# Performance work log

Hardware: AMD Instinct MI355X
Metric: run time of the kernel (lower is better)

## Reference

```python
import jax, jax.numpy as jnp
import numpy as np

H_LAT = 64   # latent height (original_shape H)
W_LAT = 64   # latent width  (original_shape W)
COND_LEN = 77  # text tokens per regional condition


def _resize_nearest_exact(m, H, W):
    # matches torch F.interpolate(mode='nearest-exact') for a 2D mask
    h0, w0 = m.shape
    ih = jnp.floor((jnp.arange(H) + 0.5) * (h0 / H)).astype(jnp.int32)
    iw = jnp.floor((jnp.arange(W) + 0.5) * (w0 / W)).astype(jnp.int32)
    return m[ih][:, iw]


def setup_inputs() -> dict:
    key = jax.random.key(0)
    kq, kk, kv, km = jax.random.split(key, 4)
    b, qlen, inner = 2, H_LAT * W_LAT, 512
    klen = 4 * COND_LEN  # 4 regions x 77 tokens
    q = jax.random.normal(kq, (b, qlen, inner), dtype=jnp.float32)
    k = jax.random.normal(kk, (b, klen, inner), dtype=jnp.float32)
    v = jax.random.normal(kv, (b, klen, inner), dtype=jnp.float32)
    dd_masks = jax.random.uniform(km, (4, 32, 32), dtype=jnp.float32)
    # ensure full spatial coverage (region 0 = global) so no softmax row is all-masked
    dd_masks = dd_masks.at[0].set(1.0)
    return {"q": q, "k": k, "v": v, "dd_masks": dd_masks, "heads": 8}


def reference(q, k, v, dd_masks, heads):
    b, qlen, inner = q.shape
    dh = inner // heads
    # [b, heads, seq, dh]
    qh = q.reshape(b, qlen, heads, dh).transpose(0, 2, 1, 3)
    kh = k.reshape(b, -1, heads, dh).transpose(0, 2, 1, 3)
    vh = v.reshape(b, -1, heads, dh).transpose(0, 2, 1, 3)

    # build DenseDiffusion mask: each region mask resized to HxW, flattened,
    # and repeated over that region's COND_LEN key columns
    R = dd_masks.shape[0]
    resized = jax.vmap(lambda m: _resize_nearest_exact(m, H_LAT, W_LAT))(dd_masks)  # [R,H,W]
    flat = resized.reshape(R, H_LAT * W_LAT).T            # [HW, R]
    masks = jnp.repeat(flat, COND_LEN, axis=1)            # [HW, R*COND_LEN]
    mask_bool = masks > 0.5                               # [HW, klen]
    mask_scale = (H_LAT * W_LAT) / jnp.sum(masks, axis=0, keepdims=True)  # [1, klen]

    scale = 1.0 / np.sqrt(dh).astype(np.float32)
    attn = jnp.einsum('bhqd,bhkd->bhqk', qh, kh) * scale  # [b,h,HW,klen]
    attn = attn * mask_scale                              # broadcast over b,h,q
    attn = jnp.where(mask_bool, attn, -jnp.inf)
    w = jax.nn.softmax(attn, axis=-1)
    out = jnp.einsum('bhqk,bhkd->bhqd', w, vh)
    return out.transpose(0, 2, 1, 3).reshape(b, qlen, heads * dh)
```

## Files before the change

### kernel.cpp

```cpp
#include <hip/hip_runtime.h>
#include <hip/hip_bf16.h>

typedef __attribute__((ext_vector_type(8))) short short8;
typedef __attribute__((ext_vector_type(4))) float floatx4;

#define HW_TOK 4096
#define KLEN 308
#define DH 64
#define INNER 512

#define KROWS 320
#define VSTRU 328
#define VBASE (KROWS * 64)
#define KV_TOTAL (VBASE + DH * VSTRU)
#define PSTR 40
#define NWAVES 16

__device__ __forceinline__ unsigned short f2bf(float f) {
    union { float f; unsigned u; } x; x.f = f;
    unsigned u = x.u;
    return (unsigned short)((u + 0x7FFFu + ((u >> 16) & 1u)) >> 16);
}
__device__ __forceinline__ unsigned pk2bf(float a, float b) {
    return ((unsigned)f2bf(b) << 16) | (unsigned)f2bf(a);
}

__global__ __launch_bounds__(1024, 1)
void dd_attn_kernel(const float* __restrict__ q,
                    const float* __restrict__ k,
                    const float* __restrict__ v,
                    const float* __restrict__ dd,
                    float* __restrict__ out) {
    __shared__ unsigned short KV[KV_TOTAL];
    __shared__ unsigned short Pb[NWAVES][16][PSTR];

    const int tid  = threadIdx.x;
    const int lane = tid & 63;
    const int wave = tid >> 6;
    const int quad = lane >> 4;
    const int l15  = lane & 15;

    const int bid = blockIdx.x;
    const int bh  = bid >> 4;
    const int grp = bid & 15;
    const int b = bh >> 3, h = bh & 7;

    const float* qp = q + (size_t)b * HW_TOK * INNER + h * DH;
    const float* kp = k + (size_t)b * KLEN * INNER + h * DH;
    const float* vp = v + (size_t)b * KLEN * INNER + h * DH;
    float* op = out + (size_t)b * HW_TOK * INNER + h * DH;

    for (int e = tid; e < KLEN * 32; e += 1024) {
        int row = e >> 5, d2 = e & 31;
        float2 f = *(const float2*)(kp + (size_t)row * INNER + 2 * d2);
        int c = d2 >> 2;
        int off = row * 64 + (((c ^ (row & 7)) << 3) | ((d2 & 3) << 1));
        *(unsigned*)&KV[off] = pk2bf(f.x, f.y);
    }
    for (int e = tid; e < 12 * 64; e += 1024) KV[KLEN * 64 + e] = 0;

    #pragma unroll
    for (int i = 0; i < 3; ++i) {
        int cq = wave + NWAVES * i;
        if (cq < 40) {
            float f[8];
            #pragma unroll
            for (int j = 0; j < 8; ++j) {
                int col = cq * 8 + j;
                f[j] = (col < KLEN) ? vp[(size_t)col * INNER + lane] : 0.f;
            }
            union { short8 s; unsigned u[4]; } vv;
            #pragma unroll
            for (int j = 0; j < 4; ++j) vv.u[j] = pk2bf(f[2 * j], f[2 * j + 1]);
            int swz = (cq & ~7) | ((cq ^ (lane & 7)) & 7);
            *(short8*)&KV[VBASE + lane * VSTRU + (swz << 3)] = vv.s;
        }
    }
    float rsum = 0.f;
    {
        const float* dp = dd + quad * 1024 + l15 * 4;
        #pragma unroll
        for (int j = 0; j < 16; ++j) {
            float4 f = *(const float4*)(dp + j * 64);
            rsum += f.x + f.y + f.z + f.w;
        }
        #pragma unroll
        for (int off = 1; off < 16; off <<= 1) rsum += __shfl_xor(rsum, off);
    }
    float rsc[4];
    #pragma unroll
    for (int r = 0; r < 4; ++r)
        rsc[r] = 4096.0f / (4.0f * __shfl(rsum, r * 16 + l15));

    __syncthreads();

    const int q0 = (grp * NWAVES + wave) * 16;
    const int qrow = q0 + l15;

    const float* qr = qp + (size_t)qrow * INNER + quad * 8;
    float4 g0 = *(const float4*)(qr);
    float4 g1 = *(const float4*)(qr + 4);
    float4 g2 = *(const float4*)(qr + 32);
    float4 g3 = *(const float4*)(qr + 36);
    short8 qa0, qa1;
    {
        union { short8 s; unsigned u[4]; } ua, ub;
        ua.u[0] = pk2bf(g0.x, g0.y); ua.u[1] = pk2bf(g0.z, g0.w);
        ua.u[2] = pk2bf(g1.x, g1.y); ua.u[3] = pk2bf(g1.z, g1.w);
        ub.u[0] = pk2bf(g2.x, g2.y); ub.u[1] = pk2bf(g2.z, g2.w);
        ub.u[2] = pk2bf(g3.x, g3.y); ub.u[3] = pk2bf(g3.z, g3.w);
        qa0 = ua.s; qa1 = ub.s;
    }

    const int mi = (qrow >> 7) * 32 + ((qrow & 63) >> 1);
    float coef[4];
    #pragma unroll
    for (int r = 0; r < 4; ++r)
        coef[r] = (dd[r * 1024 + mi] > 0.5f) ? 0.125f * rsc[r] : -1.0f;

    float m_run = -INFINITY, l_run = 0.f;
    floatx4 oacc[4] = {{0,0,0,0},{0,0,0,0},{0,0,0,0},{0,0,0,0}};

    #pragma unroll
    for (int ch = 0; ch < 4; ++ch) {
        const int NT = (ch < 3) ? 6 : 2;
        floatx4 acc[6];

        #pragma unroll
        for (int t = 0; t < NT; ++t) {
            int row = (ch * 6 + t) * 16 + l15;
            short8 ka0 = *(const short8*)&KV[row * 64 + (((quad    ) ^ (row & 7)) << 3)];
            short8 ka1 = *(const short8*)&KV[row * 64 + (((4 + quad) ^ (row & 7)) << 3)];
            floatx4 c = {0.f, 0.f, 0.f, 0.f};
            c = __builtin_amdgcn_mfma_f32_16x16x32_bf16(ka0, qa0, c, 0, 0, 0);
            c = __builtin_amdgcn_mfma_f32_16x16x32_bf16(ka1, qa1, c, 0, 0, 0);
            acc[t] = c;
        }

        float mloc = -INFINITY;
        #pragma unroll
        for (int t = 0; t < NT; ++t) {
            #pragma unroll
            for (int r = 0; r < 4; ++r) {
                int kc = (ch * 6 + t) * 16 + quad * 4 + r;
                float cf = (kc < 77) ? coef[0] : (kc < 154) ? coef[1]
                         : (kc < 231) ? coef[2] : (kc < 308) ? coef[3] : -1.0f;
                float sv = (cf > 0.f) ? acc[t][r] * cf : -INFINITY;
                acc[t][r] = sv;
                mloc = fmaxf(mloc, sv);
            }
        }
        mloc = fmaxf(mloc, __shfl_xor(mloc, 16));
        mloc = fmaxf(mloc, __shfl_xor(mloc, 32));
        float m_new = fmaxf(m_run, mloc);
        float alpha = __expf(m_run - m_new);
        float lloc = 0.f;
        #pragma unroll
        for (int t = 0; t < NT; ++t) {
            #pragma unroll
            for (int r = 0; r < 4; ++r) {
                float p = __expf(acc[t][r] - m_new);
                acc[t][r] = p;
                lloc += p;
            }
        }
        lloc += __shfl_xor(lloc, 16);
        lloc += __shfl_xor(lloc, 32);
        l_run = l_run * alpha + lloc;
        m_run = m_new;
        #pragma unroll
        for (int n = 0; n < 4; ++n)
            #pragma unroll
            for (int r = 0; r < 4; ++r) oacc[n][r] *= alpha;

        const int NS = NT / 2;
        #pragma unroll
        for (int s = 0; s < NS; ++s) {
            unsigned p0 = pk2bf(acc[2*s][0],   acc[2*s][1]);
            unsigned p1 = pk2bf(acc[2*s][2],   acc[2*s][3]);
            unsigned p2 = pk2bf(acc[2*s+1][0], acc[2*s+1][1]);
            unsigned p3 = pk2bf(acc[2*s+1][2], acc[2*s+1][3]);
            *(uint2*)&Pb[wave][l15][quad * 4]      = make_uint2(p0, p1);
            *(uint2*)&Pb[wave][l15][16 + quad * 4] = make_uint2(p2, p3);
            short8 pbv = *(const short8*)&Pb[wave][l15][quad * 8];
            #pragma unroll
            for (int n = 0; n < 4; ++n) {
                int row = n * 16 + l15;
                int cq = ch * 12 + s * 4 + quad;
                int swz = (cq & ~7) | ((cq ^ (row & 7)) & 7);
                short8 va = *(const short8*)&KV[VBASE + row * VSTRU + (swz << 3)];
                oacc[n] = __builtin_amdgcn_mfma_f32_16x16x32_bf16(va, pbv, oacc[n], 0, 0, 0);
            }
        }
    }

    const float inv = 1.0f / l_run;
    float* o = op + (size_t)qrow * INNER + quad * 4;
    #pragma unroll
    for (int n = 0; n < 4; ++n) {
        float4 ov;
        ov.x = oacc[n][0] * inv;
        ov.y = oacc[n][1] * inv;
        ov.z = oacc[n][2] * inv;
        ov.w = oacc[n][3] * inv;
        *(float4*)&o[n * 16] = ov;
    }
}

extern "C" void kernel_launch(void* const* d_in, const int* in_sizes, int n_in,
                              void* d_out, int out_size, void* d_ws, size_t ws_size,
                              hipStream_t stream) {
    const float* q  = (const float*)d_in[0];
    const float* k  = (const float*)d_in[1];
    const float* v  = (const float*)d_in[2];
    const float* dd = (const float*)d_in[3];
    float* out = (float*)d_out;
    dd_attn_kernel<<<dim3(256), dim3(1024), 0, stream>>>(q, k, v, dd, out);
}
```

Before: 93.19 us.

## Switch attention to 32x32x16 MFMA tiles with 8 waves of 32 queries

Moves both the QK^T and PV products from 16x16x32 to 32x32x16 bf16 MFMA. Each wave now handles 32 query rows and 160-key chunks (two chunks instead of four), and the block shrinks to 512 threads. The aim is fewer MFMA issues and LDS reads per unit of work, plus fewer online-softmax rescale steps and cross-lane shuffles. In exchange, per-wave register use grows (16-wide accumulators), and the last chunk computes over 12 padded zero keys. Fewer waves per block also means less latency hiding during the K/V staging.

```diff
diff --git a/kernel.cpp b/kernel.cpp
--- a/kernel.cpp
+++ b/kernel.cpp
@@ -2,7 +2,7 @@
 #include <hip/hip_bf16.h>
 
 typedef __attribute__((ext_vector_type(8))) short short8;
-typedef __attribute__((ext_vector_type(4))) float floatx4;
+typedef __attribute__((ext_vector_type(16))) float floatx16;
 
 #define HW_TOK 4096
 #define KLEN 308
@@ -13,8 +13,8 @@
 #define VSTRU 328
 #define VBASE (KROWS * 64)
 #define KV_TOTAL (VBASE + DH * VSTRU)
-#define PSTR 40
-#define NWAVES 16
+#define PSTRU 40
+#define NW 8
 
 __device__ __forceinline__ unsigned short f2bf(float f) {
     union { float f; unsigned u; } x; x.f = f;
@@ -25,18 +25,20 @@
     return ((unsigned)f2bf(b) << 16) | (unsigned)f2bf(a);
 }
 
-__global__ __launch_bounds__(1024, 1)
+__global__ __launch_bounds__(512, 1)
 void dd_attn_kernel(const float* __restrict__ q,
                     const float* __restrict__ k,
                     const float* __restrict__ v,
                     const float* __restrict__ dd,
                     float* __restrict__ out) {
     __shared__ unsigned short KV[KV_TOTAL];
-    __shared__ unsigned short Pb[NWAVES][16][PSTR];
+    __shared__ unsigned short Pb[NW][32][PSTRU];
 
     const int tid  = threadIdx.x;
     const int lane = tid & 63;
     const int wave = tid >> 6;
+    const int half = lane >> 5;
+    const int l31  = lane & 31;
     const int quad = lane >> 4;
     const int l15  = lane & 15;
 
@@ -50,31 +52,29 @@
     const float* vp = v + (size_t)b * KLEN * INNER + h * DH;
     float* op = out + (size_t)b * HW_TOK * INNER + h * DH;
 
-    for (int e = tid; e < KLEN * 32; e += 1024) {
+    for (int e = tid; e < KLEN * 32; e += 512) {
         int row = e >> 5, d2 = e & 31;
         float2 f = *(const float2*)(kp + (size_t)row * INNER + 2 * d2);
         int c = d2 >> 2;
         int off = row * 64 + (((c ^ (row & 7)) << 3) | ((d2 & 3) << 1));
         *(unsigned*)&KV[off] = pk2bf(f.x, f.y);
     }
-    for (int e = tid; e < 12 * 64; e += 1024) KV[KLEN * 64 + e] = 0;
-
-    #pragma unroll
-    for (int i = 0; i < 3; ++i) {
-        int cq = wave + NWAVES * i;
-        if (cq < 40) {
-            float f[8];
-            #pragma unroll
-            for (int j = 0; j < 8; ++j) {
-                int col = cq * 8 + j;
-                f[j] = (col < KLEN) ? vp[(size_t)col * INNER + lane] : 0.f;
-            }
-            union { short8 s; unsigned u[4]; } vv;
-            #pragma unroll
-            for (int j = 0; j < 4; ++j) vv.u[j] = pk2bf(f[2 * j], f[2 * j + 1]);
-            int swz = (cq & ~7) | ((cq ^ (lane & 7)) & 7);
-            *(short8*)&KV[VBASE + lane * VSTRU + (swz << 3)] = vv.s;
-        }
+    for (int e = tid; e < 12 * 64; e += 512) KV[KLEN * 64 + e] = 0;
+
+    #pragma unroll
+    for (int i = 0; i < 5; ++i) {
+        int cq = wave + NW * i;
+        float f[8];
+        #pragma unroll
+        for (int j = 0; j < 8; ++j) {
+            int col = cq * 8 + j;
+            f[j] = (col < KLEN) ? vp[(size_t)col * INNER + lane] : 0.f;
+        }
+        union { short8 s; unsigned u[4]; } vv;
+        #pragma unroll
+        for (int j = 0; j < 4; ++j) vv.u[j] = pk2bf(f[2 * j], f[2 * j + 1]);
+        int swz = (cq & ~7) | ((cq ^ (lane & 7)) & 7);
+        *(short8*)&KV[VBASE + lane * VSTRU + (swz << 3)] = vv.s;
     }
     float rsum = 0.f;
     {
@@ -94,22 +94,20 @@
 
     __syncthreads();
 
-    const int q0 = (grp * NWAVES + wave) * 16;
-    const int qrow = q0 + l15;
-
-    const float* qr = qp + (size_t)qrow * INNER + quad * 8;
-    float4 g0 = *(const float4*)(qr);
-    float4 g1 = *(const float4*)(qr + 4);
-    float4 g2 = *(const float4*)(qr + 32);
-    float4 g3 = *(const float4*)(qr + 36);
-    short8 qa0, qa1;
-    {
-        union { short8 s; unsigned u[4]; } ua, ub;
-        ua.u[0] = pk2bf(g0.x, g0.y); ua.u[1] = pk2bf(g0.z, g0.w);
-        ua.u[2] = pk2bf(g1.x, g1.y); ua.u[3] = pk2bf(g1.z, g1.w);
-        ub.u[0] = pk2bf(g2.x, g2.y); ub.u[1] = pk2bf(g2.z, g2.w);
-        ub.u[2] = pk2bf(g3.x, g3.y); ub.u[3] = pk2bf(g3.z, g3.w);
-        qa0 = ua.s; qa1 = ub.s;
+    const int q0 = (grp * NW + wave) * 32;
+    const int qrow = q0 + l31;
+
+    short8 qb[4];
+    const float* qr = qp + (size_t)qrow * INNER;
+    #pragma unroll
+    for (int ks = 0; ks < 4; ++ks) {
+        const float* p0 = qr + ks * 16 + half * 8;
+        float4 a = *(const float4*)p0;
+        float4 c = *(const float4*)(p0 + 4);
+        union { short8 s; unsigned u[4]; } u;
+        u.u[0] = pk2bf(a.x, a.y); u.u[1] = pk2bf(a.z, a.w);
+        u.u[2] = pk2bf(c.x, c.y); u.u[3] = pk2bf(c.z, c.w);
+        qb[ks] = u.s;
     }
 
     const int mi = (qrow >> 7) * 32 + ((qrow & 63) >> 1);
@@ -119,91 +117,113 @@
         coef[r] = (dd[r * 1024 + mi] > 0.5f) ? 0.125f * rsc[r] : -1.0f;
 
     float m_run = -INFINITY, l_run = 0.f;
-    floatx4 oacc[4] = {{0,0,0,0},{0,0,0,0},{0,0,0,0},{0,0,0,0}};
-
-    #pragma unroll
-    for (int ch = 0; ch < 4; ++ch) {
-        const int NT = (ch < 3) ? 6 : 2;
-        floatx4 acc[6];
-
-        #pragma unroll
-        for (int t = 0; t < NT; ++t) {
-            int row = (ch * 6 + t) * 16 + l15;
-            short8 ka0 = *(const short8*)&KV[row * 64 + (((quad    ) ^ (row & 7)) << 3)];
-            short8 ka1 = *(const short8*)&KV[row * 64 + (((4 + quad) ^ (row & 7)) << 3)];
-            floatx4 c = {0.f, 0.f, 0.f, 0.f};
-            c = __builtin_amdgcn_mfma_f32_16x16x32_bf16(ka0, qa0, c, 0, 0, 0);
-            c = __builtin_amdgcn_mfma_f32_16x16x32_bf16(ka1, qa1, c, 0, 0, 0);
+    floatx16 oacc[2];
+    #pragma unroll
+    for (int j = 0; j < 16; ++j) { oacc[0][j] = 0.f; oacc[1][j] = 0.f; }
+
+    #pragma unroll
+    for (int ch = 0; ch < 2; ++ch) {
+        floatx16 acc[5];
+
+        #pragma unroll
+        for (int t = 0; t < 5; ++t) {
+            int row = (ch * 5 + t) * 32 + l31;
+            floatx16 c;
+            #pragma unroll
+            for (int j = 0; j < 16; ++j) c[j] = 0.f;
+            #pragma unroll
+            for (int ks = 0; ks < 4; ++ks) {
+                int cc = ks * 2 + half;
+                short8 ka = *(const short8*)&KV[row * 64 + ((cc ^ (row & 7)) << 3)];
+                c = __builtin_amdgcn_mfma_f32_32x32x16_bf16(ka, qb[ks], c, 0, 0, 0);
+            }
             acc[t] = c;
         }
 
         float mloc = -INFINITY;
         #pragma unroll
-        for (int t = 0; t < NT; ++t) {
-            #pragma unroll
-            for (int r = 0; r < 4; ++r) {
-                int kc = (ch * 6 + t) * 16 + quad * 4 + r;
-                float cf = (kc < 77) ? coef[0] : (kc < 154) ? coef[1]
-                         : (kc < 231) ? coef[2] : (kc < 308) ? coef[3] : -1.0f;
-                float sv = (cf > 0.f) ? acc[t][r] * cf : -INFINITY;
-                acc[t][r] = sv;
-                mloc = fmaxf(mloc, sv);
-            }
-        }
-        mloc = fmaxf(mloc, __shfl_xor(mloc, 16));
+        for (int t = 0; t < 5; ++t) {
+            #pragma unroll
+            for (int reg = 0; reg < 16; ++reg) {
+                const int C0 = (ch * 5 + t) * 32 + (reg & 3) + 8 * (reg >> 2);
+                const int C1 = C0 + 4;
+                float cfA = (C0 < 77) ? coef[0] : (C0 < 154) ? coef[1]
+                          : (C0 < 231) ? coef[2] : (C0 < 308) ? coef[3] : -1.0f;
+                float cfB = (C1 < 77) ? coef[0] : (C1 < 154) ? coef[1]
+                          : (C1 < 231) ? coef[2] : (C1 < 308) ? coef[3] : -1.0f;
+                float cf = half ? cfB : cfA;
+                float sv = (cf > 0.f) ? acc[t][reg] * cf : -INFINITY;
+                acc[t][reg] = sv;
+            }
+            float m0 = fmaxf(fmaxf(acc[t][0], acc[t][1]),  fmaxf(acc[t][2], acc[t][3]));
+            float m1 = fmaxf(fmaxf(acc[t][4], acc[t][5]),  fmaxf(acc[t][6], acc[t][7]));
+            float m2 = fmaxf(fmaxf(acc[t][8], acc[t][9]),  fmaxf(acc[t][10], acc[t][11]));
+            float m3 = fmaxf(fmaxf(acc[t][12], acc[t][13]), fmaxf(acc[t][14], acc[t][15]));
+            mloc = fmaxf(mloc, fmaxf(fmaxf(m0, m1), fmaxf(m2, m3)));
+        }
         mloc = fmaxf(mloc, __shfl_xor(mloc, 32));
+
         float m_new = fmaxf(m_run, mloc);
         float alpha = __expf(m_run - m_new);
         float lloc = 0.f;
         #pragma unroll
-        for (int t = 0; t < NT; ++t) {
-            #pragma unroll
-            for (int r = 0; r < 4; ++r) {
-                float p = __expf(acc[t][r] - m_new);
-                acc[t][r] = p;
-                lloc += p;
-            }
-        }
-        lloc += __shfl_xor(lloc, 16);
+        for (int t = 0; t < 5; ++t) {
+            float s0 = 0.f, s1 = 0.f, s2 = 0.f, s3 = 0.f;
+            #pragma unroll
+            for (int g = 0; g < 4; ++g) {
+                float p0 = __expf(acc[t][4 * g]     - m_new);
+                float p1 = __expf(acc[t][4 * g + 1] - m_new);
+                float p2 = __expf(acc[t][4 * g + 2] - m_new);
+                float p3 = __expf(acc[t][4 * g + 3] - m_new);
+                acc[t][4 * g] = p0; acc[t][4 * g + 1] = p1;
+                acc[t][4 * g + 2] = p2; acc[t][4 * g + 3] = p3;
+                s0 += p0; s1 += p1; s2 += p2; s3 += p3;
+            }
+            lloc += (s0 + s1) + (s2 + s3);
+        }
         lloc += __shfl_xor(lloc, 32);
         l_run = l_run * alpha + lloc;
         m_run = m_new;
         #pragma unroll
-        for (int n = 0; n < 4; ++n)
-            #pragma unroll
-            for (int r = 0; r < 4; ++r) oacc[n][r] *= alpha;
-
-        const int NS = NT / 2;
-        #pragma unroll
-        for (int s = 0; s < NS; ++s) {
-            unsigned p0 = pk2bf(acc[2*s][0],   acc[2*s][1]);
-            unsigned p1 = pk2bf(acc[2*s][2],   acc[2*s][3]);
-            unsigned p2 = pk2bf(acc[2*s+1][0], acc[2*s+1][1]);
-            unsigned p3 = pk2bf(acc[2*s+1][2], acc[2*s+1][3]);
-            *(uint2*)&Pb[wave][l15][quad * 4]      = make_uint2(p0, p1);
-            *(uint2*)&Pb[wave][l15][16 + quad * 4] = make_uint2(p2, p3);
-            short8 pbv = *(const short8*)&Pb[wave][l15][quad * 8];
-            #pragma unroll
-            for (int n = 0; n < 4; ++n) {
-                int row = n * 16 + l15;
-                int cq = ch * 12 + s * 4 + quad;
-                int swz = (cq & ~7) | ((cq ^ (row & 7)) & 7);
-                short8 va = *(const short8*)&KV[VBASE + row * VSTRU + (swz << 3)];
-                oacc[n] = __builtin_amdgcn_mfma_f32_16x16x32_bf16(va, pbv, oacc[n], 0, 0, 0);
+        for (int j = 0; j < 16; ++j) { oacc[0][j] *= alpha; oacc[1][j] *= alpha; }
+
+        #pragma unroll
+        for (int t = 0; t < 5; ++t) {
+            #pragma unroll
+            for (int g = 0; g < 4; ++g) {
+                unsigned u0 = pk2bf(acc[t][4 * g],     acc[t][4 * g + 1]);
+                unsigned u1 = pk2bf(acc[t][4 * g + 2], acc[t][4 * g + 3]);
+                *(uint2*)&Pb[wave][l31][8 * g + 4 * half] = make_uint2(u0, u1);
+            }
+            #pragma unroll
+            for (int ks2 = 0; ks2 < 2; ++ks2) {
+                short8 pb = *(const short8*)&Pb[wave][l31][ks2 * 16 + half * 8];
+                int kc16 = (ch * 5 + t) * 2 + ks2;
+                int cc = kc16 * 2 + half;
+                #pragma unroll
+                for (int mt = 0; mt < 2; ++mt) {
+                    int vrow = 32 * mt + l31;
+                    int swz = (cc & ~7) | ((cc ^ (vrow & 7)) & 7);
+                    short8 va = *(const short8*)&KV[VBASE + vrow * VSTRU + (swz << 3)];
+                    oacc[mt] = __builtin_amdgcn_mfma_f32_32x32x16_bf16(va, pb, oacc[mt], 0, 0, 0);
+                }
             }
         }
     }
 
     const float inv = 1.0f / l_run;
-    float* o = op + (size_t)qrow * INNER + quad * 4;
-    #pragma unroll
-    for (int n = 0; n < 4; ++n) {
-        float4 ov;
-        ov.x = oacc[n][0] * inv;
-        ov.y = oacc[n][1] * inv;
-        ov.z = oacc[n][2] * inv;
-        ov.w = oacc[n][3] * inv;
-        *(float4*)&o[n * 16] = ov;
+    float* o = op + (size_t)qrow * INNER;
+    #pragma unroll
+    for (int mt = 0; mt < 2; ++mt) {
+        #pragma unroll
+        for (int g = 0; g < 4; ++g) {
+            float4 ov;
+            ov.x = oacc[mt][4 * g]     * inv;
+            ov.y = oacc[mt][4 * g + 1] * inv;
+            ov.z = oacc[mt][4 * g + 2] * inv;
+            ov.w = oacc[mt][4 * g + 3] * inv;
+            *(float4*)&o[32 * mt + 8 * g + 4 * half] = ov;
+        }
     }
 }
 
@@ -215,5 +235,5 @@
     const float* v  = (const float*)d_in[2];
     const float* dd = (const float*)d_in[3];
     float* out = (float*)d_out;
-    dd_attn_kernel<<<dim3(256), dim3(1024), 0, stream>>>(q, k, v, dd, out);
-}
+    dd_attn_kernel<<<dim3(256), dim3(512), 0, stream>>>(q, k, v, dd, out);
+}
```

After: 91.25 us. 2.1% less time.
